# Kernel optimization log

Measured on AMD Instinct MI355X. Metric: run time of the kernel, lower is better.

The kernel has to match this reference:

```python
import jax, jax.numpy as jnp
import numpy as np

N = 50000      # nodes
E = 800000     # edges (avg degree 16)
D_IN, D_H, D_OUT = 128, 128, 64
EPS = 1e-5


def setup_inputs() -> dict:
    key = jax.random.key(0)
    ks = jax.random.split(key, 6)
    feat = jax.random.normal(ks[0], (N, D_IN), dtype=jnp.float32)
    # Consistent CSR adjacency: sorted destination rows -> nodePointer via searchsorted
    rows = np.sort(np.asarray(jax.random.randint(ks[1], (E,), 0, N, dtype=jnp.int32)))
    edge_rows = jnp.asarray(rows, dtype=jnp.int32)              # [E] destination node per edge
    nodePointer = jnp.asarray(np.searchsorted(rows, np.arange(N + 1)), dtype=jnp.int32)  # [N+1]
    edgeList = jax.random.randint(ks[2], (E,), 0, N, dtype=jnp.int32)  # [E] source (column) indices
    def glorot(k, i, o):
        return jax.random.normal(k, (i, o), dtype=jnp.float32) * (1.0 / np.sqrt(i)).astype(np.float32)
    W0 = glorot(ks[3], D_IN, D_H)
    W1 = glorot(ks[4], D_H, D_H)
    W2 = glorot(ks[5], D_H, D_OUT)
    return {"feat": feat, "W0": W0, "W1": W1, "W2": W2,
            "nodePointer": nodePointer, "edgeList": edgeList, "edge_rows": edge_rows}


def _layer_norm(x):
    # Fresh nn.LayerNorm each forward in the original => weight=1, bias=0
    mu = jnp.mean(x, axis=-1, keepdims=True)
    var = jnp.mean(jnp.square(x - mu), axis=-1, keepdims=True)
    return (x - mu) * jax.lax.rsqrt(var + EPS)


def reference(feat, W0, W1, W2, nodePointer, edgeList, edge_rows):
    h = feat
    Ws = [W0, W1, W2]
    n_layers = len(Ws)
    for l, W in enumerate(Ws):
        xw = h @ W                      # [N, d_out] dense GEMM
        msg = xw[edgeList]              # [E, d_out] gather source-node features
        h = jax.ops.segment_sum(msg, edge_rows, num_segments=N)  # SpMM: A @ (h W)
        h = _layer_norm(h)
        if l != n_layers - 1:
            h = jax.nn.relu(h)
    return h
```

## Files before the change

kernel.cpp:

```cpp
#include <hip/hip_runtime.h>
#include <cstddef>


typedef __attribute__((ext_vector_type(8))) short bf16x8;
typedef __attribute__((ext_vector_type(4))) float floatx4;
typedef __attribute__((ext_vector_type(4))) unsigned int uintx4;
typedef __attribute__((ext_vector_type(2))) unsigned int uintx2;

static __device__ __forceinline__ unsigned int f2bf(float f) {
    union { float f; unsigned int u; } v; v.f = f;
    unsigned int u = v.u;
    u += 0x7fffu + ((u >> 16) & 1u);
    return u >> 16;
}
static __device__ __forceinline__ float bf_lo(unsigned int p) {
    union { unsigned int u; float f; } v; v.u = p << 16; return v.f;
}
static __device__ __forceinline__ float bf_hi(unsigned int p) {
    union { unsigned int u; float f; } v; v.u = p & 0xffff0000u; return v.f;
}

__global__ __launch_bounds__(256) void cvt_feat(const float* __restrict__ in,
                                                unsigned int* __restrict__ out,
                                                int n8) {
    int i = blockIdx.x * 256 + threadIdx.x;
    if (i < n8) {
        float4 a = ((const float4*)in)[i * 2];
        float4 b = ((const float4*)in)[i * 2 + 1];
        uintx4 p;
        p.x = (f2bf(a.y) << 16) | f2bf(a.x);
        p.y = (f2bf(a.w) << 16) | f2bf(a.z);
        p.z = (f2bf(b.y) << 16) | f2bf(b.x);
        p.w = (f2bf(b.w) << 16) | f2bf(b.z);
        ((uintx4*)out)[i] = p;
    }
}

__global__ __launch_bounds__(256) void cvt_w(const float* __restrict__ W0,
                                             const float* __restrict__ W1,
                                             const float* __restrict__ W2,
                                             unsigned int* __restrict__ Wt) {
    const int m = blockIdx.x >> 4;
    const int slice = blockIdx.x & 15;
    const float* W = (m == 0) ? W0 : (m == 1) ? W1 : W2;
    const int ncols = (m == 2) ? 64 : 128;
    unsigned int* dst = Wt + m * 128 * 64;
    const int total = ncols * 64;
    for (int idx = slice * 256 + threadIdx.x; idx < total; idx += 16 * 256) {
        int kk = idx / ncols;
        int n  = idx - kk * ncols;
        unsigned int lo = f2bf(W[(size_t)(2 * kk) * ncols + n]);
        unsigned int hi = f2bf(W[(size_t)(2 * kk + 1) * ncols + n]);
        dst[(size_t)n * 64 + kk] = (hi << 16) | lo;
    }
}

template <int NCOLS>
__global__ __launch_bounds__(64) void gemm_mfma(const unsigned int* __restrict__ A,
                                                const unsigned int* __restrict__ Wt,
                                                unsigned int* __restrict__ C,
                                                int M) {
    const int lane = threadIdx.x;
    const int row0 = blockIdx.x * 16;
    const int quad = lane >> 4;
    const int mcol = lane & 15;
    const int arow_idx = row0 + mcol;
    const int aload = (arow_idx < M) ? arow_idx : (M - 1);

    constexpr int NT = NCOLS / 16;
    floatx4 acc[NT];
    #pragma unroll
    for (int t = 0; t < NT; ++t) acc[t] = (floatx4){0.f, 0.f, 0.f, 0.f};

    const unsigned int* arow = A + (size_t)aload * 64 + quad * 4;

    #pragma unroll
    for (int k0 = 0; k0 < 128; k0 += 32) {
        uintx4 ap = *(const uintx4*)(arow + k0 / 2);
        bf16x8 a = __builtin_bit_cast(bf16x8, ap);

        const int koff = (k0 + quad * 8) >> 1;
        #pragma unroll
        for (int t = 0; t < NT; ++t) {
            const unsigned int* brow = Wt + (size_t)(t * 16 + mcol) * 64 + koff;
            uintx4 bp = *(const uintx4*)brow;
            bf16x8 b = __builtin_bit_cast(bf16x8, bp);
            acc[t] = __builtin_amdgcn_mfma_f32_16x16x32_bf16(a, b, acc[t], 0, 0, 0);
        }
    }

    const int rowStride = NCOLS >> 1;
    #pragma unroll
    for (int t = 0; t < NT; ++t) {
        #pragma unroll
        for (int r = 0; r < 4; ++r) {
            unsigned int mybf = f2bf(acc[t][r]);
            unsigned int pair = __shfl_xor(mybf, 1, 64);
            int orow = row0 + quad * 4 + r;
            if (orow < M && (mcol & 1) == 0) {
                unsigned int packed = (pair << 16) | mybf;
                C[(size_t)orow * rowStride + t * 8 + (mcol >> 1)] = packed;
            }
        }
    }
}

__global__ __launch_bounds__(256) void agg_ln128(const unsigned int* __restrict__ xw,
                                                 const int* __restrict__ ptr,
                                                 const int* __restrict__ col,
                                                 unsigned int* __restrict__ out,
                                                 int N) {
    const int node = blockIdx.x * 4 + (threadIdx.x >> 6);
    if (node >= N) return;
    const int lane = threadIdx.x & 63;
    const int g  = lane >> 4;
    const int sl = lane & 15;
    const int s = ptr[node];
    const int e = ptr[node + 1];

    float accA[8] = {}, accB[8] = {};
    const unsigned int* base = xw + sl * 4;
    int i = s + g;
    for (; i + 4 < e; i += 8) {
        uintx4 v0 = *(const uintx4*)(base + (size_t)col[i] * 64);
        uintx4 v1 = *(const uintx4*)(base + (size_t)col[i + 4] * 64);
        accA[0] += bf_lo(v0.x); accA[1] += bf_hi(v0.x);
        accA[2] += bf_lo(v0.y); accA[3] += bf_hi(v0.y);
        accA[4] += bf_lo(v0.z); accA[5] += bf_hi(v0.z);
        accA[6] += bf_lo(v0.w); accA[7] += bf_hi(v0.w);
        accB[0] += bf_lo(v1.x); accB[1] += bf_hi(v1.x);
        accB[2] += bf_lo(v1.y); accB[3] += bf_hi(v1.y);
        accB[4] += bf_lo(v1.z); accB[5] += bf_hi(v1.z);
        accB[6] += bf_lo(v1.w); accB[7] += bf_hi(v1.w);
    }
    if (i < e) {
        uintx4 v0 = *(const uintx4*)(base + (size_t)col[i] * 64);
        accA[0] += bf_lo(v0.x); accA[1] += bf_hi(v0.x);
        accA[2] += bf_lo(v0.y); accA[3] += bf_hi(v0.y);
        accA[4] += bf_lo(v0.z); accA[5] += bf_hi(v0.z);
        accA[6] += bf_lo(v0.w); accA[7] += bf_hi(v0.w);
    }

    float acc[8];
    #pragma unroll
    for (int j = 0; j < 8; ++j) acc[j] = accA[j] + accB[j];

    #pragma unroll
    for (int j = 0; j < 8; ++j) {
        acc[j] += __shfl_xor(acc[j], 16, 64);
        acc[j] += __shfl_xor(acc[j], 32, 64);
    }
    float s1 = 0.f, s2 = 0.f;
    #pragma unroll
    for (int j = 0; j < 8; ++j) { s1 += acc[j]; s2 += acc[j] * acc[j]; }
    #pragma unroll
    for (int m = 8; m >= 1; m >>= 1) {
        s1 += __shfl_xor(s1, m, 64);
        s2 += __shfl_xor(s2, m, 64);
    }
    const float mean = s1 * (1.0f / 128.0f);
    const float var  = s2 * (1.0f / 128.0f) - mean * mean;
    const float inv  = rsqrtf(var + 1e-5f);

    if (g == 0) {
        float o[8];
        #pragma unroll
        for (int j = 0; j < 8; ++j)
            o[j] = fmaxf((acc[j] - mean) * inv, 0.f);
        uintx4 p;
        p.x = (f2bf(o[1]) << 16) | f2bf(o[0]);
        p.y = (f2bf(o[3]) << 16) | f2bf(o[2]);
        p.z = (f2bf(o[5]) << 16) | f2bf(o[4]);
        p.w = (f2bf(o[7]) << 16) | f2bf(o[6]);
        *(uintx4*)(out + (size_t)node * 64 + sl * 4) = p;
    }
}

__global__ __launch_bounds__(256) void agg_ln64(const unsigned int* __restrict__ xw,
                                                const int* __restrict__ ptr,
                                                const int* __restrict__ col,
                                                float* __restrict__ out, int N) {
    const int node = blockIdx.x * 4 + (threadIdx.x >> 6);
    if (node >= N) return;
    const int lane = threadIdx.x & 63;
    const int g  = lane >> 4;
    const int sl = lane & 15;
    const int s = ptr[node];
    const int e = ptr[node + 1];

    float accA[4] = {}, accB[4] = {};
    const unsigned int* base = xw + sl * 2;
    int i = s + g;
    for (; i + 4 < e; i += 8) {
        uintx2 v0 = *(const uintx2*)(base + (size_t)col[i] * 32);
        uintx2 v1 = *(const uintx2*)(base + (size_t)col[i + 4] * 32);
        accA[0] += bf_lo(v0.x); accA[1] += bf_hi(v0.x);
        accA[2] += bf_lo(v0.y); accA[3] += bf_hi(v0.y);
        accB[0] += bf_lo(v1.x); accB[1] += bf_hi(v1.x);
        accB[2] += bf_lo(v1.y); accB[3] += bf_hi(v1.y);
    }
    if (i < e) {
        uintx2 v0 = *(const uintx2*)(base + (size_t)col[i] * 32);
        accA[0] += bf_lo(v0.x); accA[1] += bf_hi(v0.x);
        accA[2] += bf_lo(v0.y); accA[3] += bf_hi(v0.y);
    }

    float acc[4];
    #pragma unroll
    for (int j = 0; j < 4; ++j) acc[j] = accA[j] + accB[j];

    #pragma unroll
    for (int j = 0; j < 4; ++j) {
        acc[j] += __shfl_xor(acc[j], 16, 64);
        acc[j] += __shfl_xor(acc[j], 32, 64);
    }
    float s1 = 0.f, s2 = 0.f;
    #pragma unroll
    for (int j = 0; j < 4; ++j) { s1 += acc[j]; s2 += acc[j] * acc[j]; }
    #pragma unroll
    for (int m = 8; m >= 1; m >>= 1) {
        s1 += __shfl_xor(s1, m, 64);
        s2 += __shfl_xor(s2, m, 64);
    }
    const float mean = s1 * (1.0f / 64.0f);
    const float var  = s2 * (1.0f / 64.0f) - mean * mean;
    const float inv  = rsqrtf(var + 1e-5f);

    if (g == 0) {
        float4 o;
        o.x = (acc[0] - mean) * inv;
        o.y = (acc[1] - mean) * inv;
        o.z = (acc[2] - mean) * inv;
        o.w = (acc[3] - mean) * inv;
        *(float4*)(out + (size_t)node * 64 + sl * 4) = o;
    }
}

extern "C" void kernel_launch(void* const* d_in, const int* in_sizes, int n_in,
                              void* d_out, int out_size, void* d_ws, size_t ws_size,
                              hipStream_t stream) {
    const float* feat = (const float*)d_in[0];
    const float* W0   = (const float*)d_in[1];
    const float* W1   = (const float*)d_in[2];
    const float* W2   = (const float*)d_in[3];
    const int*   ptr  = (const int*)d_in[4];
    const int*   col  = (const int*)d_in[5];

    const int N = in_sizes[4] - 1;

    unsigned int* xwp = (unsigned int*)d_ws;
    unsigned int* hb  = xwp + (size_t)N * 64;
    unsigned int* fb  = hb + (size_t)N * 64;
    unsigned int* WtP = fb + (size_t)N * 64;
    float*        out = (float*)d_out;

    const int gemmBlocks = (N + 15) / 16;
    const int nodeBlocks = (N + 3) / 4;

    cvt_feat<<<(N * 16 + 255) / 256, 256, 0, stream>>>(feat, fb, N * 16);
    cvt_w<<<48, 256, 0, stream>>>(W0, W1, W2, WtP);

    gemm_mfma<128><<<gemmBlocks, 64, 0, stream>>>(fb, WtP, xwp, N);
    agg_ln128<<<nodeBlocks, 256, 0, stream>>>(xwp, ptr, col, hb, N);
    gemm_mfma<128><<<gemmBlocks, 64, 0, stream>>>(hb, WtP + 128 * 64, xwp, N);
    agg_ln128<<<nodeBlocks, 256, 0, stream>>>(xwp, ptr, col, hb, N);
    gemm_mfma<64><<<gemmBlocks, 64, 0, stream>>>(hb, WtP + 2 * 128 * 64, xwp, N);
    agg_ln64<<<nodeBlocks, 256, 0, stream>>>(xwp, ptr, col, out, N);
}
```

Measured before the change: 227.8 us.

## Fuse all GCN layers into one persistent cooperative kernel with grid syncs

Replaces the eight separate launches (conversions, three GEMMs, three aggregations) with a single cooperative persistent kernel that walks through the phases in grid-stride loops, separated by grid-wide barriers. The aim is to remove per-launch overhead and the gaps between kernels. In exchange, occupancy is capped at a fixed resident grid (up to 4 blocks per CU, with 256 CUs assumed). The GEMM now runs per wave over 64-column halves, and grid.sync barriers can stall while the irregular aggregation phases finish.

Measured after the change: 706.2 us. +209.9%, slower.

```diff
diff --git a/kernel.cpp b/kernel.cpp
--- a/kernel.cpp
+++ b/kernel.cpp
@@ -1,5 +1,8 @@
 #include <hip/hip_runtime.h>
+#include <hip/hip_cooperative_groups.h>
 #include <cstddef>
+
+namespace cg = cooperative_groups;
 
 
 typedef __attribute__((ext_vector_type(8))) short bf16x8;
@@ -20,220 +23,247 @@
     union { unsigned int u; float f; } v; v.u = p & 0xffff0000u; return v.f;
 }
 
-__global__ __launch_bounds__(256) void cvt_feat(const float* __restrict__ in,
-                                                unsigned int* __restrict__ out,
-                                                int n8) {
-    int i = blockIdx.x * 256 + threadIdx.x;
-    if (i < n8) {
-        float4 a = ((const float4*)in)[i * 2];
-        float4 b = ((const float4*)in)[i * 2 + 1];
-        uintx4 p;
-        p.x = (f2bf(a.y) << 16) | f2bf(a.x);
-        p.y = (f2bf(a.w) << 16) | f2bf(a.z);
-        p.z = (f2bf(b.y) << 16) | f2bf(b.x);
-        p.w = (f2bf(b.w) << 16) | f2bf(b.z);
-        ((uintx4*)out)[i] = p;
-    }
-}
-
-__global__ __launch_bounds__(256) void cvt_w(const float* __restrict__ W0,
-                                             const float* __restrict__ W1,
-                                             const float* __restrict__ W2,
-                                             unsigned int* __restrict__ Wt) {
-    const int m = blockIdx.x >> 4;
-    const int slice = blockIdx.x & 15;
-    const float* W = (m == 0) ? W0 : (m == 1) ? W1 : W2;
-    const int ncols = (m == 2) ? 64 : 128;
-    unsigned int* dst = Wt + m * 128 * 64;
-    const int total = ncols * 64;
-    for (int idx = slice * 256 + threadIdx.x; idx < total; idx += 16 * 256) {
-        int kk = idx / ncols;
-        int n  = idx - kk * ncols;
-        unsigned int lo = f2bf(W[(size_t)(2 * kk) * ncols + n]);
-        unsigned int hi = f2bf(W[(size_t)(2 * kk + 1) * ncols + n]);
-        dst[(size_t)n * 64 + kk] = (hi << 16) | lo;
-    }
-}
-
 template <int NCOLS>
-__global__ __launch_bounds__(64) void gemm_mfma(const unsigned int* __restrict__ A,
-                                                const unsigned int* __restrict__ Wt,
-                                                unsigned int* __restrict__ C,
-                                                int M) {
-    const int lane = threadIdx.x;
-    const int row0 = blockIdx.x * 16;
+static __device__ __forceinline__ void gemm_phase(const unsigned int* __restrict__ A,
+                                                  const unsigned int* __restrict__ Wt,
+                                                  unsigned int* __restrict__ C,
+                                                  int M, int gwave, int nWaves) {
+    const int lane = threadIdx.x & 63;
     const int quad = lane >> 4;
     const int mcol = lane & 15;
-    const int arow_idx = row0 + mcol;
-    const int aload = (arow_idx < M) ? arow_idx : (M - 1);
-
-    constexpr int NT = NCOLS / 16;
-    floatx4 acc[NT];
-    #pragma unroll
-    for (int t = 0; t < NT; ++t) acc[t] = (floatx4){0.f, 0.f, 0.f, 0.f};
-
-    const unsigned int* arow = A + (size_t)aload * 64 + quad * 4;
-
-    #pragma unroll
-    for (int k0 = 0; k0 < 128; k0 += 32) {
-        uintx4 ap = *(const uintx4*)(arow + k0 / 2);
-        bf16x8 a = __builtin_bit_cast(bf16x8, ap);
-
-        const int koff = (k0 + quad * 8) >> 1;
+    constexpr int HALVES = NCOLS / 64;
+    const int rowTiles = (M + 15) >> 4;
+    const int totalTiles = rowTiles * HALVES;
+    const int rowStride = NCOLS >> 1;
+
+    for (int t = gwave; t < totalTiles; t += nWaves) {
+        const int rowTile = (HALVES == 2) ? (t >> 1) : t;
+        const int half    = (HALVES == 2) ? (t & 1) : 0;
+        const int row0 = rowTile * 16;
+        int aidx = row0 + mcol; if (aidx >= M) aidx = M - 1;
+        const unsigned int* arow = A + (size_t)aidx * 64 + quad * 4;
+        const unsigned int* WtH  = Wt + (size_t)half * 64 * 64;
+
+        floatx4 acc[4];
         #pragma unroll
-        for (int t = 0; t < NT; ++t) {
-            const unsigned int* brow = Wt + (size_t)(t * 16 + mcol) * 64 + koff;
-            uintx4 bp = *(const uintx4*)brow;
-            bf16x8 b = __builtin_bit_cast(bf16x8, bp);
-            acc[t] = __builtin_amdgcn_mfma_f32_16x16x32_bf16(a, b, acc[t], 0, 0, 0);
+        for (int tt = 0; tt < 4; ++tt) acc[tt] = (floatx4){0.f, 0.f, 0.f, 0.f};
+
+        #pragma unroll
+        for (int k0 = 0; k0 < 128; k0 += 32) {
+            uintx4 ap = *(const uintx4*)(arow + k0 / 2);
+            bf16x8 a = __builtin_bit_cast(bf16x8, ap);
+            const int koff = (k0 + quad * 8) >> 1;
+            #pragma unroll
+            for (int tt = 0; tt < 4; ++tt) {
+                const unsigned int* brow = WtH + (size_t)(tt * 16 + mcol) * 64 + koff;
+                uintx4 bp = *(const uintx4*)brow;
+                bf16x8 b = __builtin_bit_cast(bf16x8, bp);
+                acc[tt] = __builtin_amdgcn_mfma_f32_16x16x32_bf16(a, b, acc[tt], 0, 0, 0);
+            }
+        }
+        #pragma unroll
+        for (int tt = 0; tt < 4; ++tt) {
+            #pragma unroll
+            for (int r = 0; r < 4; ++r) {
+                unsigned int mybf = f2bf(acc[tt][r]);
+                unsigned int pair = __shfl_xor(mybf, 1, 64);
+                int orow = row0 + quad * 4 + r;
+                if (orow < M && (mcol & 1) == 0) {
+                    unsigned int packed = (pair << 16) | mybf;
+                    C[(size_t)orow * rowStride + half * 32 + tt * 8 + (mcol >> 1)] = packed;
+                }
+            }
         }
     }
-
-    const int rowStride = NCOLS >> 1;
-    #pragma unroll
-    for (int t = 0; t < NT; ++t) {
-        #pragma unroll
-        for (int r = 0; r < 4; ++r) {
-            unsigned int mybf = f2bf(acc[t][r]);
-            unsigned int pair = __shfl_xor(mybf, 1, 64);
-            int orow = row0 + quad * 4 + r;
-            if (orow < M && (mcol & 1) == 0) {
-                unsigned int packed = (pair << 16) | mybf;
-                C[(size_t)orow * rowStride + t * 8 + (mcol >> 1)] = packed;
-            }
-        }
-    }
-}
-
-__global__ __launch_bounds__(256) void agg_ln128(const unsigned int* __restrict__ xw,
-                                                 const int* __restrict__ ptr,
-                                                 const int* __restrict__ col,
-                                                 unsigned int* __restrict__ out,
-                                                 int N) {
-    const int node = blockIdx.x * 4 + (threadIdx.x >> 6);
-    if (node >= N) return;
+}
+
+static __device__ __forceinline__ void agg128_phase(const unsigned int* __restrict__ xw,
+                                                    const int* __restrict__ ptr,
+                                                    const int* __restrict__ col,
+                                                    unsigned int* __restrict__ out,
+                                                    int N) {
     const int lane = threadIdx.x & 63;
+    const int wv = threadIdx.x >> 6;
     const int g  = lane >> 4;
     const int sl = lane & 15;
-    const int s = ptr[node];
-    const int e = ptr[node + 1];
-
-    float accA[8] = {}, accB[8] = {};
     const unsigned int* base = xw + sl * 4;
-    int i = s + g;
-    for (; i + 4 < e; i += 8) {
-        uintx4 v0 = *(const uintx4*)(base + (size_t)col[i] * 64);
-        uintx4 v1 = *(const uintx4*)(base + (size_t)col[i + 4] * 64);
-        accA[0] += bf_lo(v0.x); accA[1] += bf_hi(v0.x);
-        accA[2] += bf_lo(v0.y); accA[3] += bf_hi(v0.y);
-        accA[4] += bf_lo(v0.z); accA[5] += bf_hi(v0.z);
-        accA[6] += bf_lo(v0.w); accA[7] += bf_hi(v0.w);
-        accB[0] += bf_lo(v1.x); accB[1] += bf_hi(v1.x);
-        accB[2] += bf_lo(v1.y); accB[3] += bf_hi(v1.y);
-        accB[4] += bf_lo(v1.z); accB[5] += bf_hi(v1.z);
-        accB[6] += bf_lo(v1.w); accB[7] += bf_hi(v1.w);
+
+    for (int nb = blockIdx.x; nb * 4 < N; nb += gridDim.x) {
+        const int node = nb * 4 + wv;
+        if (node < N) {
+            const int s = ptr[node];
+            const int e = ptr[node + 1];
+            float accA[8] = {}, accB[8] = {};
+            int i = s + g;
+            for (; i + 4 < e; i += 8) {
+                uintx4 v0 = *(const uintx4*)(base + (size_t)col[i] * 64);
+                uintx4 v1 = *(const uintx4*)(base + (size_t)col[i + 4] * 64);
+                accA[0] += bf_lo(v0.x); accA[1] += bf_hi(v0.x);
+                accA[2] += bf_lo(v0.y); accA[3] += bf_hi(v0.y);
+                accA[4] += bf_lo(v0.z); accA[5] += bf_hi(v0.z);
+                accA[6] += bf_lo(v0.w); accA[7] += bf_hi(v0.w);
+                accB[0] += bf_lo(v1.x); accB[1] += bf_hi(v1.x);
+                accB[2] += bf_lo(v1.y); accB[3] += bf_hi(v1.y);
+                accB[4] += bf_lo(v1.z); accB[5] += bf_hi(v1.z);
+                accB[6] += bf_lo(v1.w); accB[7] += bf_hi(v1.w);
+            }
+            if (i < e) {
+                uintx4 v0 = *(const uintx4*)(base + (size_t)col[i] * 64);
+                accA[0] += bf_lo(v0.x); accA[1] += bf_hi(v0.x);
+                accA[2] += bf_lo(v0.y); accA[3] += bf_hi(v0.y);
+                accA[4] += bf_lo(v0.z); accA[5] += bf_hi(v0.z);
+                accA[6] += bf_lo(v0.w); accA[7] += bf_hi(v0.w);
+            }
+            float acc[8];
+            #pragma unroll
+            for (int j = 0; j < 8; ++j) acc[j] = accA[j] + accB[j];
+            #pragma unroll
+            for (int j = 0; j < 8; ++j) {
+                acc[j] += __shfl_xor(acc[j], 16, 64);
+                acc[j] += __shfl_xor(acc[j], 32, 64);
+            }
+            float s1 = 0.f, s2 = 0.f;
+            #pragma unroll
+            for (int j = 0; j < 8; ++j) { s1 += acc[j]; s2 += acc[j] * acc[j]; }
+            #pragma unroll
+            for (int m = 8; m >= 1; m >>= 1) {
+                s1 += __shfl_xor(s1, m, 64);
+                s2 += __shfl_xor(s2, m, 64);
+            }
+            const float mean = s1 * (1.0f / 128.0f);
+            const float var  = s2 * (1.0f / 128.0f) - mean * mean;
+            const float inv  = rsqrtf(var + 1e-5f);
+            if (g == 0) {
+                float o[8];
+                #pragma unroll
+                for (int j = 0; j < 8; ++j)
+                    o[j] = fmaxf((acc[j] - mean) * inv, 0.f);
+                uintx4 p;
+                p.x = (f2bf(o[1]) << 16) | f2bf(o[0]);
+                p.y = (f2bf(o[3]) << 16) | f2bf(o[2]);
+                p.z = (f2bf(o[5]) << 16) | f2bf(o[4]);
+                p.w = (f2bf(o[7]) << 16) | f2bf(o[6]);
+                *(uintx4*)(out + (size_t)node * 64 + sl * 4) = p;
+            }
+        }
     }
-    if (i < e) {
-        uintx4 v0 = *(const uintx4*)(base + (size_t)col[i] * 64);
-        accA[0] += bf_lo(v0.x); accA[1] += bf_hi(v0.x);
-        accA[2] += bf_lo(v0.y); accA[3] += bf_hi(v0.y);
-        accA[4] += bf_lo(v0.z); accA[5] += bf_hi(v0.z);
-        accA[6] += bf_lo(v0.w); accA[7] += bf_hi(v0.w);
-    }
-
-    float acc[8];
-    #pragma unroll
-    for (int j = 0; j < 8; ++j) acc[j] = accA[j] + accB[j];
-
-    #pragma unroll
-    for (int j = 0; j < 8; ++j) {
-        acc[j] += __shfl_xor(acc[j], 16, 64);
-        acc[j] += __shfl_xor(acc[j], 32, 64);
-    }
-    float s1 = 0.f, s2 = 0.f;
-    #pragma unroll
-    for (int j = 0; j < 8; ++j) { s1 += acc[j]; s2 += acc[j] * acc[j]; }
-    #pragma unroll
-    for (int m = 8; m >= 1; m >>= 1) {
-        s1 += __shfl_xor(s1, m, 64);
-        s2 += __shfl_xor(s2, m, 64);
-    }
-    const float mean = s1 * (1.0f / 128.0f);
-    const float var  = s2 * (1.0f / 128.0f) - mean * mean;
-    const float inv  = rsqrtf(var + 1e-5f);
-
-    if (g == 0) {
-        float o[8];
-        #pragma unroll
-        for (int j = 0; j < 8; ++j)
-            o[j] = fmaxf((acc[j] - mean) * inv, 0.f);
-        uintx4 p;
-        p.x = (f2bf(o[1]) << 16) | f2bf(o[0]);
-        p.y = (f2bf(o[3]) << 16) | f2bf(o[2]);
-        p.z = (f2bf(o[5]) << 16) | f2bf(o[4]);
-        p.w = (f2bf(o[7]) << 16) | f2bf(o[6]);
-        *(uintx4*)(out + (size_t)node * 64 + sl * 4) = p;
-    }
-}
-
-__global__ __launch_bounds__(256) void agg_ln64(const unsigned int* __restrict__ xw,
-                                                const int* __restrict__ ptr,
-                                                const int* __restrict__ col,
-                                                float* __restrict__ out, int N) {
-    const int node = blockIdx.x * 4 + (threadIdx.x >> 6);
-    if (node >= N) return;
+}
+
+static __device__ __forceinline__ void agg64_phase(const unsigned int* __restrict__ xw,
+                                                   const int* __restrict__ ptr,
+                                                   const int* __restrict__ col,
+                                                   float* __restrict__ out, int N) {
     const int lane = threadIdx.x & 63;
+    const int wv = threadIdx.x >> 6;
     const int g  = lane >> 4;
     const int sl = lane & 15;
-    const int s = ptr[node];
-    const int e = ptr[node + 1];
-
-    float accA[4] = {}, accB[4] = {};
     const unsigned int* base = xw + sl * 2;
-    int i = s + g;
-    for (; i + 4 < e; i += 8) {
-        uintx2 v0 = *(const uintx2*)(base + (size_t)col[i] * 32);
-        uintx2 v1 = *(const uintx2*)(base + (size_t)col[i + 4] * 32);
-        accA[0] += bf_lo(v0.x); accA[1] += bf_hi(v0.x);
-        accA[2] += bf_lo(v0.y); accA[3] += bf_hi(v0.y);
-        accB[0] += bf_lo(v1.x); accB[1] += bf_hi(v1.x);
-        accB[2] += bf_lo(v1.y); accB[3] += bf_hi(v1.y);
+
+    for (int nb = blockIdx.x; nb * 4 < N; nb += gridDim.x) {
+        const int node = nb * 4 + wv;
+        if (node < N) {
+            const int s = ptr[node];
+            const int e = ptr[node + 1];
+            float accA[4] = {}, accB[4] = {};
+            int i = s + g;
+            for (; i + 4 < e; i += 8) {
+                uintx2 v0 = *(const uintx2*)(base + (size_t)col[i] * 32);
+                uintx2 v1 = *(const uintx2*)(base + (size_t)col[i + 4] * 32);
+                accA[0] += bf_lo(v0.x); accA[1] += bf_hi(v0.x);
+                accA[2] += bf_lo(v0.y); accA[3] += bf_hi(v0.y);
+                accB[0] += bf_lo(v1.x); accB[1] += bf_hi(v1.x);
+                accB[2] += bf_lo(v1.y); accB[3] += bf_hi(v1.y);
+            }
+            if (i < e) {
+                uintx2 v0 = *(const uintx2*)(base + (size_t)col[i] * 32);
+                accA[0] += bf_lo(v0.x); accA[1] += bf_hi(v0.x);
+                accA[2] += bf_lo(v0.y); accA[3] += bf_hi(v0.y);
+            }
+            float acc[4];
+            #pragma unroll
+            for (int j = 0; j < 4; ++j) acc[j] = accA[j] + accB[j];
+            #pragma unroll
+            for (int j = 0; j < 4; ++j) {
+                acc[j] += __shfl_xor(acc[j], 16, 64);
+                acc[j] += __shfl_xor(acc[j], 32, 64);
+            }
+            float s1 = 0.f, s2 = 0.f;
+            #pragma unroll
+            for (int j = 0; j < 4; ++j) { s1 += acc[j]; s2 += acc[j] * acc[j]; }
+            #pragma unroll
+            for (int m = 8; m >= 1; m >>= 1) {
+                s1 += __shfl_xor(s1, m, 64);
+                s2 += __shfl_xor(s2, m, 64);
+            }
+            const float mean = s1 * (1.0f / 64.0f);
+            const float var  = s2 * (1.0f / 64.0f) - mean * mean;
+            const float inv  = rsqrtf(var + 1e-5f);
+            if (g == 0) {
+                float4 o;
+                o.x = (acc[0] - mean) * inv;
+                o.y = (acc[1] - mean) * inv;
+                o.z = (acc[2] - mean) * inv;
+                o.w = (acc[3] - mean) * inv;
+                *(float4*)(out + (size_t)node * 64 + sl * 4) = o;
+            }
+        }
     }
-    if (i < e) {
-        uintx2 v0 = *(const uintx2*)(base + (size_t)col[i] * 32);
-        accA[0] += bf_lo(v0.x); accA[1] += bf_hi(v0.x);
-        accA[2] += bf_lo(v0.y); accA[3] += bf_hi(v0.y);
+}
+
+__global__ __launch_bounds__(256, 4) void gcn_fused(
+    const float* __restrict__ feat, const float* __restrict__ W0,
+    const float* __restrict__ W1, const float* __restrict__ W2,
+    const int* __restrict__ ptr, const int* __restrict__ col,
+    unsigned int* __restrict__ xwp, unsigned int* __restrict__ hb,
+    unsigned int* __restrict__ fb, unsigned int* __restrict__ WtP,
+    float* __restrict__ out, int N)
+{
+    cg::grid_group grid = cg::this_grid();
+    const int gtid = blockIdx.x * 256 + threadIdx.x;
+    const int nThreads = gridDim.x * 256;
+    const int gwave = blockIdx.x * 4 + (threadIdx.x >> 6);
+    const int nWaves = gridDim.x * 4;
+
+    {
+        const int n8 = N * 16;
+        for (int i = gtid; i < n8; i += nThreads) {
+            float4 a = ((const float4*)feat)[i * 2];
+            float4 b = ((const float4*)feat)[i * 2 + 1];
+            uintx4 p;
+            p.x = (f2bf(a.y) << 16) | f2bf(a.x);
+            p.y = (f2bf(a.w) << 16) | f2bf(a.z);
+            p.z = (f2bf(b.y) << 16) | f2bf(b.x);
+            p.w = (f2bf(b.w) << 16) | f2bf(b.z);
+            ((uintx4*)fb)[i] = p;
+        }
+        #pragma unroll
+        for (int m = 0; m < 3; ++m) {
+            const float* W = (m == 0) ? W0 : (m == 1) ? W1 : W2;
+            const int ncols = (m == 2) ? 64 : 128;
+            unsigned int* dst = WtP + m * 128 * 64;
+            const int total = ncols * 64;
+            for (int idx = gtid; idx < total; idx += nThreads) {
+                int kk = idx / ncols;
+                int n  = idx - kk * ncols;
+                unsigned int lo = f2bf(W[(size_t)(2 * kk) * ncols + n]);
+                unsigned int hi = f2bf(W[(size_t)(2 * kk + 1) * ncols + n]);
+                dst[(size_t)n * 64 + kk] = (hi << 16) | lo;
+            }
+        }
     }
-
-    float acc[4];
-    #pragma unroll
-    for (int j = 0; j < 4; ++j) acc[j] = accA[j] + accB[j];
-
-    #pragma unroll
-    for (int j = 0; j < 4; ++j) {
-        acc[j] += __shfl_xor(acc[j], 16, 64);
-        acc[j] += __shfl_xor(acc[j], 32, 64);
-    }
-    float s1 = 0.f, s2 = 0.f;
-    #pragma unroll
-    for (int j = 0; j < 4; ++j) { s1 += acc[j]; s2 += acc[j] * acc[j]; }
-    #pragma unroll
-    for (int m = 8; m >= 1; m >>= 1) {
-        s1 += __shfl_xor(s1, m, 64);
-        s2 += __shfl_xor(s2, m, 64);
-    }
-    const float mean = s1 * (1.0f / 64.0f);
-    const float var  = s2 * (1.0f / 64.0f) - mean * mean;
-    const float inv  = rsqrtf(var + 1e-5f);
-
-    if (g == 0) {
-        float4 o;
-        o.x = (acc[0] - mean) * inv;
-        o.y = (acc[1] - mean) * inv;
-        o.z = (acc[2] - mean) * inv;
-        o.w = (acc[3] - mean) * inv;
-        *(float4*)(out + (size_t)node * 64 + sl * 4) = o;
-    }
+    grid.sync();
+
+    gemm_phase<128>(fb, WtP, xwp, N, gwave, nWaves);
+    grid.sync();
+    agg128_phase(xwp, ptr, col, hb, N);
+    grid.sync();
+    gemm_phase<128>(hb, WtP + 128 * 64, xwp, N, gwave, nWaves);
+    grid.sync();
+    agg128_phase(xwp, ptr, col, hb, N);
+    grid.sync();
+    gemm_phase<64>(hb, WtP + 2 * 128 * 64, xwp, N, gwave, nWaves);
+    grid.sync();
+    agg64_phase(xwp, ptr, col, out, N);
 }
 
 extern "C" void kernel_launch(void* const* d_in, const int* in_sizes, int n_in,
@@ -246,7 +276,7 @@
     const int*   ptr  = (const int*)d_in[4];
     const int*   col  = (const int*)d_in[5];
 
-    const int N = in_sizes[4] - 1;
+    int N = in_sizes[4] - 1;
 
     unsigned int* xwp = (unsigned int*)d_ws;
     unsigned int* hb  = xwp + (size_t)N * 64;
@@ -254,16 +284,20 @@
     unsigned int* WtP = fb + (size_t)N * 64;
     float*        out = (float*)d_out;
 
-    const int gemmBlocks = (N + 15) / 16;
-    const int nodeBlocks = (N + 3) / 4;
-
-    cvt_feat<<<(N * 16 + 255) / 256, 256, 0, stream>>>(feat, fb, N * 16);
-    cvt_w<<<48, 256, 0, stream>>>(W0, W1, W2, WtP);
-
-    gemm_mfma<128><<<gemmBlocks, 64, 0, stream>>>(fb, WtP, xwp, N);
-    agg_ln128<<<nodeBlocks, 256, 0, stream>>>(xwp, ptr, col, hb, N);
-    gemm_mfma<128><<<gemmBlocks, 64, 0, stream>>>(hb, WtP + 128 * 64, xwp, N);
-    agg_ln128<<<nodeBlocks, 256, 0, stream>>>(xwp, ptr, col, hb, N);
-    gemm_mfma<64><<<gemmBlocks, 64, 0, stream>>>(hb, WtP + 2 * 128 * 64, xwp, N);
-    agg_ln64<<<nodeBlocks, 256, 0, stream>>>(xwp, ptr, col, out, N);
-}
+    int maxB = 0;
+    if (hipOccupancyMaxActiveBlocksPerMultiprocessor(
+            &maxB, reinterpret_cast<const void*>(gcn_fused), 256, 0) != hipSuccess ||
+        maxB <= 0)
+        maxB = 2;
+    if (maxB > 4) maxB = 4;
+    dim3 gridDim(maxB * 256), blockDim(256);
+
+    void* args[] = {
+        (void*)&feat, (void*)&W0, (void*)&W1, (void*)&W2,
+        (void*)&ptr, (void*)&col,
+        (void*)&xwp, (void*)&hb, (void*)&fb, (void*)&WtP,
+        (void*)&out, (void*)&N
+    };
+    hipLaunchCooperativeKernel(reinterpret_cast<void*>(gcn_fused),
+                               gridDim, blockDim, args, 0, stream);
+}
```

## Fuse fp32-to-bf16 feature conversion into first GEMM and unroll gather loops deeper

Applied to the files above, without the earlier changes.

Removes the standalone cvt_feat kernel; the first GEMM now reads fp32 features directly and converts to bf16 in registers before the MFMA. This drops one launch and a write plus read of the bf16 feature copy. The aggregation kernels also unroll the neighbor gather to four outstanding loads per iteration for more memory-level parallelism, at some cost in register pressure.

Result: faster. 223.3 us (-2.0%).

```diff
diff --git a/kernel.cpp b/kernel.cpp
--- a/kernel.cpp
+++ b/kernel.cpp
@@ -19,21 +19,15 @@
 static __device__ __forceinline__ float bf_hi(unsigned int p) {
     union { unsigned int u; float f; } v; v.u = p & 0xffff0000u; return v.f;
 }
-
-__global__ __launch_bounds__(256) void cvt_feat(const float* __restrict__ in,
-                                                unsigned int* __restrict__ out,
-                                                int n8) {
-    int i = blockIdx.x * 256 + threadIdx.x;
-    if (i < n8) {
-        float4 a = ((const float4*)in)[i * 2];
-        float4 b = ((const float4*)in)[i * 2 + 1];
-        uintx4 p;
-        p.x = (f2bf(a.y) << 16) | f2bf(a.x);
-        p.y = (f2bf(a.w) << 16) | f2bf(a.z);
-        p.z = (f2bf(b.y) << 16) | f2bf(b.x);
-        p.w = (f2bf(b.w) << 16) | f2bf(b.z);
-        ((uintx4*)out)[i] = p;
-    }
+static __device__ __forceinline__ void acc8(float* a, uintx4 v) {
+    a[0] += bf_lo(v.x); a[1] += bf_hi(v.x);
+    a[2] += bf_lo(v.y); a[3] += bf_hi(v.y);
+    a[4] += bf_lo(v.z); a[5] += bf_hi(v.z);
+    a[6] += bf_lo(v.w); a[7] += bf_hi(v.w);
+}
+static __device__ __forceinline__ void acc4(float* a, uintx2 v) {
+    a[0] += bf_lo(v.x); a[1] += bf_hi(v.x);
+    a[2] += bf_lo(v.y); a[3] += bf_hi(v.y);
 }
 
 __global__ __launch_bounds__(256) void cvt_w(const float* __restrict__ W0,
@@ -55,8 +49,8 @@
     }
 }
 
-template <int NCOLS>
-__global__ __launch_bounds__(64) void gemm_mfma(const unsigned int* __restrict__ A,
+template <int NCOLS, bool A_FP32>
+__global__ __launch_bounds__(64) void gemm_mfma(const void* __restrict__ Av,
                                                 const unsigned int* __restrict__ Wt,
                                                 unsigned int* __restrict__ C,
                                                 int M) {
@@ -64,20 +58,32 @@
     const int row0 = blockIdx.x * 16;
     const int quad = lane >> 4;
     const int mcol = lane & 15;
-    const int arow_idx = row0 + mcol;
-    const int aload = (arow_idx < M) ? arow_idx : (M - 1);
+    int aidx = row0 + mcol; if (aidx >= M) aidx = M - 1;
 
     constexpr int NT = NCOLS / 16;
     floatx4 acc[NT];
     #pragma unroll
     for (int t = 0; t < NT; ++t) acc[t] = (floatx4){0.f, 0.f, 0.f, 0.f};
 
-    const unsigned int* arow = A + (size_t)aload * 64 + quad * 4;
+    const float*        arowF = (const float*)Av + (size_t)aidx * 128 + quad * 8;
+    const unsigned int* arowB = (const unsigned int*)Av + (size_t)aidx * 64 + quad * 4;
 
     #pragma unroll
     for (int k0 = 0; k0 < 128; k0 += 32) {
-        uintx4 ap = *(const uintx4*)(arow + k0 / 2);
-        bf16x8 a = __builtin_bit_cast(bf16x8, ap);
+        bf16x8 a;
+        if constexpr (A_FP32) {
+            float4 fa = *(const float4*)(arowF + k0);
+            float4 fb = *(const float4*)(arowF + k0 + 4);
+            uintx4 ap;
+            ap.x = (f2bf(fa.y) << 16) | f2bf(fa.x);
+            ap.y = (f2bf(fa.w) << 16) | f2bf(fa.z);
+            ap.z = (f2bf(fb.y) << 16) | f2bf(fb.x);
+            ap.w = (f2bf(fb.w) << 16) | f2bf(fb.z);
+            a = __builtin_bit_cast(bf16x8, ap);
+        } else {
+            uintx4 ap = *(const uintx4*)(arowB + k0 / 2);
+            a = __builtin_bit_cast(bf16x8, ap);
+        }
 
         const int koff = (k0 + quad * 8) >> 1;
         #pragma unroll
@@ -121,24 +127,16 @@
     float accA[8] = {}, accB[8] = {};
     const unsigned int* base = xw + sl * 4;
     int i = s + g;
-    for (; i + 4 < e; i += 8) {
+    for (; i + 12 < e; i += 16) {
+        uintx4 v0 = *(const uintx4*)(base + (size_t)col[i]      * 64);
+        uintx4 v1 = *(const uintx4*)(base + (size_t)col[i + 4]  * 64);
+        uintx4 v2 = *(const uintx4*)(base + (size_t)col[i + 8]  * 64);
+        uintx4 v3 = *(const uintx4*)(base + (size_t)col[i + 12] * 64);
+        acc8(accA, v0); acc8(accB, v1); acc8(accA, v2); acc8(accB, v3);
+    }
+    for (; i < e; i += 4) {
         uintx4 v0 = *(const uintx4*)(base + (size_t)col[i] * 64);
-        uintx4 v1 = *(const uintx4*)(base + (size_t)col[i + 4] * 64);
-        accA[0] += bf_lo(v0.x); accA[1] += bf_hi(v0.x);
-        accA[2] += bf_lo(v0.y); accA[3] += bf_hi(v0.y);
-        accA[4] += bf_lo(v0.z); accA[5] += bf_hi(v0.z);
-        accA[6] += bf_lo(v0.w); accA[7] += bf_hi(v0.w);
-        accB[0] += bf_lo(v1.x); accB[1] += bf_hi(v1.x);
-        accB[2] += bf_lo(v1.y); accB[3] += bf_hi(v1.y);
-        accB[4] += bf_lo(v1.z); accB[5] += bf_hi(v1.z);
-        accB[6] += bf_lo(v1.w); accB[7] += bf_hi(v1.w);
-    }
-    if (i < e) {
-        uintx4 v0 = *(const uintx4*)(base + (size_t)col[i] * 64);
-        accA[0] += bf_lo(v0.x); accA[1] += bf_hi(v0.x);
-        accA[2] += bf_lo(v0.y); accA[3] += bf_hi(v0.y);
-        accA[4] += bf_lo(v0.z); accA[5] += bf_hi(v0.z);
-        accA[6] += bf_lo(v0.w); accA[7] += bf_hi(v0.w);
+        acc8(accA, v0);
     }
 
     float acc[8];
@@ -191,18 +189,16 @@
     float accA[4] = {}, accB[4] = {};
     const unsigned int* base = xw + sl * 2;
     int i = s + g;
-    for (; i + 4 < e; i += 8) {
+    for (; i + 12 < e; i += 16) {
+        uintx2 v0 = *(const uintx2*)(base + (size_t)col[i]      * 32);
+        uintx2 v1 = *(const uintx2*)(base + (size_t)col[i + 4]  * 32);
+        uintx2 v2 = *(const uintx2*)(base + (size_t)col[i + 8]  * 32);
+        uintx2 v3 = *(const uintx2*)(base + (size_t)col[i + 12] * 32);
+        acc4(accA, v0); acc4(accB, v1); acc4(accA, v2); acc4(accB, v3);
+    }
+    for (; i < e; i += 4) {
         uintx2 v0 = *(const uintx2*)(base + (size_t)col[i] * 32);
-        uintx2 v1 = *(const uintx2*)(base + (size_t)col[i + 4] * 32);
-        accA[0] += bf_lo(v0.x); accA[1] += bf_hi(v0.x);
-        accA[2] += bf_lo(v0.y); accA[3] += bf_hi(v0.y);
-        accB[0] += bf_lo(v1.x); accB[1] += bf_hi(v1.x);
-        accB[2] += bf_lo(v1.y); accB[3] += bf_hi(v1.y);
-    }
-    if (i < e) {
-        uintx2 v0 = *(const uintx2*)(base + (size_t)col[i] * 32);
-        accA[0] += bf_lo(v0.x); accA[1] += bf_hi(v0.x);
-        accA[2] += bf_lo(v0.y); accA[3] += bf_hi(v0.y);
+        acc4(accA, v0);
     }
 
     float acc[4];
@@ -250,20 +246,18 @@
 
     unsigned int* xwp = (unsigned int*)d_ws;
     unsigned int* hb  = xwp + (size_t)N * 64;
-    unsigned int* fb  = hb + (size_t)N * 64;
-    unsigned int* WtP = fb + (size_t)N * 64;
+    unsigned int* WtP = hb + (size_t)N * 64;
     float*        out = (float*)d_out;
 
     const int gemmBlocks = (N + 15) / 16;
     const int nodeBlocks = (N + 3) / 4;
 
-    cvt_feat<<<(N * 16 + 255) / 256, 256, 0, stream>>>(feat, fb, N * 16);
     cvt_w<<<48, 256, 0, stream>>>(W0, W1, W2, WtP);
 
-    gemm_mfma<128><<<gemmBlocks, 64, 0, stream>>>(fb, WtP, xwp, N);
+    gemm_mfma<128, true><<<gemmBlocks, 64, 0, stream>>>(feat, WtP, xwp, N);
     agg_ln128<<<nodeBlocks, 256, 0, stream>>>(xwp, ptr, col, hb, N);
-    gemm_mfma<128><<<gemmBlocks, 64, 0, stream>>>(hb, WtP + 128 * 64, xwp, N);
+    gemm_mfma<128, false><<<gemmBlocks, 64, 0, stream>>>(hb, WtP + 128 * 64, xwp, N);
     agg_ln128<<<nodeBlocks, 256, 0, stream>>>(xwp, ptr, col, hb, N);
-    gemm_mfma<64><<<gemmBlocks, 64, 0, stream>>>(hb, WtP + 2 * 128 * 64, xwp, N);
+    gemm_mfma<64, false><<<gemmBlocks, 64, 0, stream>>>(hb, WtP + 2 * 128 * 64, xwp, N);
     agg_ln64<<<nodeBlocks, 256, 0, stream>>>(xwp, ptr, col, out, N);
 }
```
